# Optimization experiments

Hardware: AMD Instinct MI355X
Metric: run time of the kernel (lower is better)

Reference implementation:

```python
import jax, jax.numpy as jnp
import numpy as np

B, L, V, D = 16384, 200, 1000000, 20
PAD_FRAC = 0.3


def setup_inputs() -> dict:
    key = jax.random.key(0)
    k_ids, k_pad, k_emb = jax.random.split(key, 3)
    inputs = jax.random.randint(k_ids, (B, L), 0, V, dtype=jnp.int64)
    pad = jax.random.uniform(k_pad, (B, L)) < PAD_FRAC
    inputs = jnp.where(pad, 0, inputs)
    emb_table = jax.random.normal(k_emb, (V, D), dtype=jnp.float32)
    emb_table = emb_table.at[0].set(0.0)  # padding_idx=0 -> zero row
    return {"inputs": inputs, "emb_table": emb_table}


def reference(inputs, emb_table):
    # Embedding gather: [B, L, D]
    emb = emb_table[inputs]
    # Row filter: keep rows whose embedding sum != 0 (non-padding)
    keep = (emb.sum(axis=-1) != 0)  # [B, L] bool
    cnt = keep.sum(axis=-1)         # [B]
    pooled = (emb * keep[..., None].astype(emb.dtype)).sum(axis=1)  # [B, D]
    pooled = pooled / jnp.maximum(cnt, 1)[:, None].astype(emb.dtype)
    # Fallback: all rows filtered -> zeros(D)
    return jnp.where((cnt > 0)[:, None], pooled, jnp.zeros((), emb.dtype))
```

## Files before the change

kernel.cpp:

```cpp
#include <hip/hip_runtime.h>

static constexpr int B = 16384;
static constexpr int L = 200;
static constexpr int D = 20;

__global__ __launch_bounds__(256) void wd_pool_kernel(
    const int* __restrict__ ids,
    const float* __restrict__ emb,
    float* __restrict__ out)
{
    const int lane = threadIdx.x & 63;
    const int row  = (blockIdx.x << 2) + (threadIdx.x >> 6);

    const int* __restrict__ rid = ids + (size_t)row * L;

    float a[D];
#pragma unroll
    for (int i = 0; i < D; ++i) a[i] = 0.0f;
    float cntf = 0.0f;

    for (int t = lane; t < L; t += 64) {
        const int id = rid[t];
        if (id != 0) {
            const float4* __restrict__ r =
                (const float4*)(emb + (size_t)id * D);
            float4 v[5];
#pragma unroll
            for (int q = 0; q < 5; ++q) v[q] = r[q];

            float s = 0.0f;
#pragma unroll
            for (int q = 0; q < 5; ++q) s += (v[q].x + v[q].y) + (v[q].z + v[q].w);

            const float k = (s != 0.0f) ? 1.0f : 0.0f;
#pragma unroll
            for (int q = 0; q < 5; ++q) {
                a[4 * q + 0] += v[q].x * k;
                a[4 * q + 1] += v[q].y * k;
                a[4 * q + 2] += v[q].z * k;
                a[4 * q + 3] += v[q].w * k;
            }
            cntf += k;
        }
    }

#pragma unroll
    for (int off = 32; off; off >>= 1) {
#pragma unroll
        for (int i = 0; i < D; ++i) a[i] += __shfl_xor(a[i], off, 64);
        cntf += __shfl_xor(cntf, off, 64);
    }

    if (lane == 0) {
        const float inv = 1.0f / fmaxf(cntf, 1.0f);
        float4* __restrict__ o = (float4*)(out + (size_t)row * D);
#pragma unroll
        for (int q = 0; q < 5; ++q) {
            float4 w;
            w.x = a[4 * q + 0] * inv;
            w.y = a[4 * q + 1] * inv;
            w.z = a[4 * q + 2] * inv;
            w.w = a[4 * q + 3] * inv;
            o[q] = w;
        }
    }
}

extern "C" void kernel_launch(void* const* d_in, const int* in_sizes, int n_in,
                              void* d_out, int out_size, void* d_ws, size_t ws_size,
                              hipStream_t stream) {
    const int*   ids = (const int*)d_in[0];
    const float* emb = (const float*)d_in[1];
    float*       out = (float*)d_out;

    dim3 grid(B / 4);
    dim3 block(256);
    hipLaunchKernelGGL(wd_pool_kernel, grid, block, 0, stream, ids, emb, out);
}
```

Baseline: 71.95 us.

## Split each embedding row across five lanes and issue all gathers up front

Changes the thread mapping so that five lanes cooperatively load one 80-byte embedding row, each taking one float4. Token ids are distributed across lanes with shuffles. All 17 gather loads are issued back-to-back through inline asm before a single waitcnt, which raises memory-level parallelism and coalescing per wavefront. Per-row sums and the final reduction use cross-lane shuffles, so there are more shuffle instructions. Padding rows are no longer skipped; they load row 0 instead, and 4 of the 64 lanes sit idle.

```diff
diff --git a/kernel.cpp b/kernel.cpp
--- a/kernel.cpp
+++ b/kernel.cpp
@@ -3,6 +3,10 @@
 static constexpr int B = 16384;
 static constexpr int L = 200;
 static constexpr int D = 20;
+static constexpr int TPG = 12;
+static constexpr int NG  = (L + TPG - 1) / TPG;
+
+typedef float f32x4 __attribute__((ext_vector_type(4)));
 
 __global__ __launch_bounds__(256) void wd_pool_kernel(
     const int* __restrict__ ids,
@@ -11,58 +15,83 @@
 {
     const int lane = threadIdx.x & 63;
     const int row  = (blockIdx.x << 2) + (threadIdx.x >> 6);
-
     const int* __restrict__ rid = ids + (size_t)row * L;
 
-    float a[D];
+    const int s = lane / 5;
+    const int c = lane - 5 * s;
+
+    int idv0 = rid[lane];
+    int idv1 = rid[lane + 64];
+    int idv2 = rid[lane + 128];
+    int idv3 = (lane + 192 < L) ? rid[lane + 192] : 0;
+
+    f32x4 v[NG];
 #pragma unroll
-    for (int i = 0; i < D; ++i) a[i] = 0.0f;
-    float cntf = 0.0f;
+    for (int g = 0; g < NG; ++g) {
+        const int t  = TPG * g + s;
+        const int tl = t & 63;
+        const int jlo = (TPG * g) >> 6;
+        const int jhi = (TPG * g + TPG) >> 6;
+        int vlo = (jlo == 0) ? idv0 : (jlo == 1) ? idv1 : (jlo == 2) ? idv2 : idv3;
+        int idt = __shfl(vlo, tl, 64);
+        if (jhi != jlo) {
+            int vhi = (jhi == 1) ? idv1 : (jhi == 2) ? idv2 : idv3;
+            int hi  = __shfl(vhi, tl, 64);
+            idt = ((t >> 6) == jhi) ? hi : idt;
+        }
+        const bool tvalid = (t < L) && (lane < 60);
+        idt = tvalid ? idt : 0;
 
-    for (int t = lane; t < L; t += 64) {
-        const int id = rid[t];
-        if (id != 0) {
-            const float4* __restrict__ r =
-                (const float4*)(emb + (size_t)id * D);
-            float4 v[5];
-#pragma unroll
-            for (int q = 0; q < 5; ++q) v[q] = r[q];
-
-            float s = 0.0f;
-#pragma unroll
-            for (int q = 0; q < 5; ++q) s += (v[q].x + v[q].y) + (v[q].z + v[q].w);
-
-            const float k = (s != 0.0f) ? 1.0f : 0.0f;
-#pragma unroll
-            for (int q = 0; q < 5; ++q) {
-                a[4 * q + 0] += v[q].x * k;
-                a[4 * q + 1] += v[q].y * k;
-                a[4 * q + 2] += v[q].z * k;
-                a[4 * q + 3] += v[q].w * k;
-            }
-            cntf += k;
-        }
+        const float* p = emb + (size_t)idt * D + 4 * c;
+        asm volatile("global_load_dwordx4 %0, %1, off" : "=v"(v[g]) : "v"(p));
     }
 
+    asm volatile("s_waitcnt vmcnt(0)"
+                 : "+v"(v[0]), "+v"(v[1]), "+v"(v[2]), "+v"(v[3]), "+v"(v[4]),
+                   "+v"(v[5]), "+v"(v[6]), "+v"(v[7]), "+v"(v[8]), "+v"(v[9]),
+                   "+v"(v[10]), "+v"(v[11]), "+v"(v[12]), "+v"(v[13]), "+v"(v[14]),
+                   "+v"(v[15]), "+v"(v[16]));
+
+    float a0 = 0.f, a1 = 0.f, a2 = 0.f, a3 = 0.f, cntf = 0.f;
+    const int gb = 5 * s;
 #pragma unroll
-    for (int off = 32; off; off >>= 1) {
-#pragma unroll
-        for (int i = 0; i < D; ++i) a[i] += __shfl_xor(a[i], off, 64);
-        cntf += __shfl_xor(cntf, off, 64);
+    for (int g = 0; g < NG; ++g) {
+        const int t = TPG * g + s;
+        const float ps = (v[g][0] + v[g][1]) + (v[g][2] + v[g][3]);
+        const float S = ((__shfl(ps, gb, 64) + __shfl(ps, gb + 1, 64)) +
+                         (__shfl(ps, gb + 2, 64) + __shfl(ps, gb + 3, 64))) +
+                        __shfl(ps, gb + 4, 64);
+        const bool tvalid = (t < L) && (lane < 60);
+        const float k = (S != 0.0f && tvalid) ? 1.0f : 0.0f;
+        a0 += v[g][0] * k;
+        a1 += v[g][1] * k;
+        a2 += v[g][2] * k;
+        a3 += v[g][3] * k;
+        cntf += k;
     }
 
-    if (lane == 0) {
+    {
+        a0 += __shfl(a0, lane + 30, 64); a1 += __shfl(a1, lane + 30, 64);
+        a2 += __shfl(a2, lane + 30, 64); a3 += __shfl(a3, lane + 30, 64);
+        cntf += __shfl(cntf, lane + 30, 64);
+
+        a0 += __shfl(a0, lane + 15, 64); a1 += __shfl(a1, lane + 15, 64);
+        a2 += __shfl(a2, lane + 15, 64); a3 += __shfl(a3, lane + 15, 64);
+        cntf += __shfl(cntf, lane + 15, 64);
+
+        float b0 = __shfl(a0, lane + 5, 64) + __shfl(a0, lane + 10, 64);
+        float b1 = __shfl(a1, lane + 5, 64) + __shfl(a1, lane + 10, 64);
+        float b2 = __shfl(a2, lane + 5, 64) + __shfl(a2, lane + 10, 64);
+        float b3 = __shfl(a3, lane + 5, 64) + __shfl(a3, lane + 10, 64);
+        float bc = __shfl(cntf, lane + 5, 64) + __shfl(cntf, lane + 10, 64);
+        a0 += b0; a1 += b1; a2 += b2; a3 += b3; cntf += bc;
+    }
+
+    if (lane < 5) {
         const float inv = 1.0f / fmaxf(cntf, 1.0f);
-        float4* __restrict__ o = (float4*)(out + (size_t)row * D);
-#pragma unroll
-        for (int q = 0; q < 5; ++q) {
-            float4 w;
-            w.x = a[4 * q + 0] * inv;
-            w.y = a[4 * q + 1] * inv;
-            w.z = a[4 * q + 2] * inv;
-            w.w = a[4 * q + 3] * inv;
-            o[q] = w;
-        }
+        float4 w;
+        w.x = a0 * inv; w.y = a1 * inv; w.z = a2 * inv; w.w = a3 * inv;
+        *(float4*)(out + (size_t)row * D + 4 * lane) = w;
     }
 }
 
```

After: 65.14 us. -9.5%, faster.
